# Performance work log

Hardware: AMD Instinct MI355X
Metric: run time of the kernel (lower is better)

Reference implementation:

```python
import jax, jax.numpy as jnp
import numpy as np

RADIUS = 5
WIN = (RADIUS - 1) * 2 + 1  # 9


def setup_inputs() -> dict:
    key = jax.random.key(0)
    k1, k2 = jax.random.split(key)
    B, K, H, W = 4, 4, 224, 224
    seg = jax.random.uniform(k1, (B, K, H, W), dtype=jnp.float32)
    weight = jax.random.uniform(k2, (B, 1, H, W, WIN, WIN), dtype=jnp.float32)
    return {"seg": seg, "weight": weight}


def reference(seg, weight):
    # seg: [B,K,H,W]; weight: [B,1,H,W,w,w] local affinity window, w = 2*(radius-1)+1
    B, K, H, W = seg.shape
    Kconst = jnp.float32(K)
    # torch pads by `radius` on all sides but only uses window offsets 0..2*(radius-1),
    # i.e. relative offsets [-radius, radius-2] -- replicate exactly.
    padded = jnp.pad(seg, ((0, 0), (0, 0), (RADIUS, RADIUS), (RADIUS, RADIUS)))
    # weighted sum over the local window without materializing [B,K,H,W,w,w]
    sum_w_seg = jnp.zeros_like(seg)
    for m in range(WIN):
        for n in range(WIN):
            sum_w_seg = sum_w_seg + padded[:, :, m:m + H, n:n + W] * weight[:, :, :, :, m, n]
    assocA = jnp.sum(sum_w_seg * seg, axis=(-1, -2))                      # [B,K]
    assocV = jnp.sum(jnp.sum(weight, axis=(-1, -2)) * seg, axis=(-1, -2))  # [B,K]
    assoc = jnp.sum(assocA / assocV, axis=-1)                              # [B]
    return jnp.sum(Kconst - assoc)
```

## Files before the change

### kernel.cpp

```cpp
#include <hip/hip_runtime.h>

#define RADIUS 5
#define WIN 9
#define BB 4
#define KK 4
#define HH 224
#define WW 224
#define HW (HH * WW)
#define PD 234
#define PAREA (PD * PD)
#define NBUCKET 64
#define PARTIAL_FLOATS (NBUCKET * BB * 8)

#define PX_PER_BLOCK 64
#define BLOCKS_TOTAL (BB * HW / PX_PER_BLOCK)
#define WF4_PER_BLOCK (PX_PER_BLOCK * 81 / 4)


__global__ __launch_bounds__(256) void ncuts_pad(
    const float* __restrict__ seg, float4* __restrict__ pseg)
{
    const int tid = blockIdx.x * 256 + threadIdx.x;
    if (tid >= BB * PAREA) return;
    const int b  = tid / PAREA;
    const int rc = tid - b * PAREA;
    const int r  = rc / PD;
    const int c  = rc - r * PD;
    const int hh = r - RADIUS;
    const int ww = c - RADIUS;
    float4 v = {0.f, 0.f, 0.f, 0.f};
    if (hh >= 0 && hh < HH && ww >= 0 && ww < WW) {
        const float* sb = seg + (size_t)b * KK * HW + hh * WW + ww;
        v.x = sb[0 * HW];
        v.y = sb[1 * HW];
        v.z = sb[2 * HW];
        v.w = sb[3 * HW];
    }
    pseg[tid] = v;
}

template<int T0, int T1>
__device__ __forceinline__ void do_taps(const float* __restrict__ wl,
                                        const float4* __restrict__ pb, int roff,
                                        float& a0, float& a1, float& a2, float& a3,
                                        float& wsum)
{
    #pragma unroll
    for (int tap = T0; tap < T1; ++tap) {
        const int m = tap / 9;
        const int n = tap - 9 * m;
        const float wv = wl[tap];
        const float4 s = pb[roff + m * PD + n];
        a0 = fmaf(wv, s.x, a0);
        a1 = fmaf(wv, s.y, a1);
        a2 = fmaf(wv, s.z, a2);
        a3 = fmaf(wv, s.w, a3);
        wsum += wv;
    }
}

__global__ __launch_bounds__(256, 7) void ncuts_main(
    const float4* __restrict__ weight4,
    const float4* __restrict__ pseg,
    float* __restrict__ partial)
{
    __shared__ float wlds[PX_PER_BLOCK * 81];

    const int tid  = threadIdx.x;
    const int lane = tid & 63;
    const int ws   = tid >> 6;

    const float4* wsrc = weight4 + (size_t)blockIdx.x * WF4_PER_BLOCK;
    float4* wdst = (float4*)wlds;
    #pragma unroll
    for (int it = 0; it < 6; ++it) {
        const int idx = it * 256 + tid;
        if (idx < WF4_PER_BLOCK) wdst[idx] = wsrc[idx];
    }
    __syncthreads();

    const int px  = blockIdx.x * PX_PER_BLOCK + lane;
    const int b   = px / HW;
    const int rem = px - b * HW;
    const int h   = rem / WW;
    const int w   = rem - h * WW;
    const int roff = h * PD + w;

    const float4* pb = pseg + (size_t)b * PAREA;
    const float* wl  = &wlds[lane * 81];

    float a0 = 0.f, a1 = 0.f, a2 = 0.f, a3 = 0.f, wsum = 0.f;

    switch (ws) {
        case 0: do_taps< 0, 21>(wl, pb, roff, a0, a1, a2, a3, wsum); break;
        case 1: do_taps<21, 41>(wl, pb, roff, a0, a1, a2, a3, wsum); break;
        case 2: do_taps<41, 61>(wl, pb, roff, a0, a1, a2, a3, wsum); break;
        default: do_taps<61, 81>(wl, pb, roff, a0, a1, a2, a3, wsum); break;
    }

    const float4 o = pb[roff + RADIUS * PD + RADIUS];

    float vals[8] = { a0 * o.x, a1 * o.y, a2 * o.z, a3 * o.w,
                      wsum * o.x, wsum * o.y, wsum * o.z, wsum * o.w };

    #pragma unroll
    for (int i = 0; i < 8; ++i) {
        float v = vals[i];
        v += __shfl_down(v, 32);
        v += __shfl_down(v, 16);
        v += __shfl_down(v, 8);
        v += __shfl_down(v, 4);
        v += __shfl_down(v, 2);
        v += __shfl_down(v, 1);
        vals[i] = v;
    }

    if (lane == 0) {
        const int bucket = (blockIdx.x * 4 + ws) & (NBUCKET - 1);
        float* dst = partial + (bucket * BB + b) * 8;
        #pragma unroll
        for (int i = 0; i < 8; ++i)
            atomicAdd(dst + i, vals[i]);
    }
}

__global__ __launch_bounds__(64) void ncuts_final(
    const float* __restrict__ partial, float* __restrict__ out)
{
    __shared__ float sums[32];
    const int t = threadIdx.x;
    if (t < 32) {
        const int b = t >> 3;
        const int i = t & 7;
        float s = 0.f;
        for (int bucket = 0; bucket < NBUCKET; ++bucket)
            s += partial[(bucket * BB + b) * 8 + i];
        sums[b * 8 + i] = s;
    }
    __syncthreads();
    if (t == 0) {
        float total = 0.f;
        for (int b = 0; b < BB; ++b) {
            float assoc = 0.f;
            for (int k = 0; k < KK; ++k) {
                const float A = sums[b * 8 + k];
                const float V = sums[b * 8 + 4 + k];
                assoc += A / V;
            }
            total += (float)KK - assoc;
        }
        out[0] = total;
    }
}

extern "C" void kernel_launch(void* const* d_in, const int* in_sizes, int n_in,
                              void* d_out, int out_size, void* d_ws, size_t ws_size,
                              hipStream_t stream) {
    const float* seg     = (const float*)d_in[0];
    const float4* weight = (const float4*)d_in[1];
    float* out     = (float*)d_out;
    float* wsf     = (float*)d_ws;
    float* partial = wsf;
    float4* pseg   = (float4*)(wsf + PARTIAL_FLOATS);

    hipMemsetAsync(d_ws, 0, PARTIAL_FLOATS * sizeof(float), stream);

    {
        const int total = BB * PAREA;
        const int grid  = (total + 255) / 256;
        hipLaunchKernelGGL(ncuts_pad, dim3(grid), dim3(256), 0, stream, seg, pseg);
    }
    {
        hipLaunchKernelGGL(ncuts_main, dim3(BLOCKS_TOTAL), dim3(256), 0, stream,
                           weight, pseg, partial);
    }
    hipLaunchKernelGGL(ncuts_final, dim3(1), dim3(64), 0, stream, partial, out);
}
```

Baseline: 123.0 us.

## Fuse memset and final reduction into pad/main kernels; load weights via global_load_lds

Replaces the hipMemsetAsync with zeroing of the partial and counter buffers inside the pad kernel. The final reduction kernel becomes a last-block-done step in the main kernel, driven by an atomic counter and thread fences. Weight tiles are staged into LDS with direct global-to-LDS loads, which skip the register round trip. This cuts two launches or stream operations and some load overhead, at the cost of an extra atomic and fence in every block.

```diff
diff --git a/kernel.cpp b/kernel.cpp
--- a/kernel.cpp
+++ b/kernel.cpp
@@ -11,16 +11,19 @@
 #define PAREA (PD * PD)
 #define NBUCKET 64
 #define PARTIAL_FLOATS (NBUCKET * BB * 8)
+#define CTRL_FLOATS 2056
+#define PSEG_OFF 2560
 
 #define PX_PER_BLOCK 64
 #define BLOCKS_TOTAL (BB * HW / PX_PER_BLOCK)
 #define WF4_PER_BLOCK (PX_PER_BLOCK * 81 / 4)
 
-
 __global__ __launch_bounds__(256) void ncuts_pad(
-    const float* __restrict__ seg, float4* __restrict__ pseg)
+    const float* __restrict__ seg, float4* __restrict__ pseg,
+    float* __restrict__ ctrl)
 {
     const int tid = blockIdx.x * 256 + threadIdx.x;
+    if (tid < CTRL_FLOATS) ctrl[tid] = 0.0f;
     if (tid >= BB * PAREA) return;
     const int b  = tid / PAREA;
     const int rc = tid - b * PAREA;
@@ -62,21 +65,30 @@
 __global__ __launch_bounds__(256, 7) void ncuts_main(
     const float4* __restrict__ weight4,
     const float4* __restrict__ pseg,
-    float* __restrict__ partial)
+    float* __restrict__ partial,
+    int* __restrict__ counter,
+    float* __restrict__ out)
 {
     __shared__ float wlds[PX_PER_BLOCK * 81];
+    __shared__ float xred[32];
+    __shared__ int lastflag;
 
     const int tid  = threadIdx.x;
     const int lane = tid & 63;
     const int ws   = tid >> 6;
 
     const float4* wsrc = weight4 + (size_t)blockIdx.x * WF4_PER_BLOCK;
-    float4* wdst = (float4*)wlds;
+    float4* wlds4 = (float4*)wlds;
     #pragma unroll
-    for (int it = 0; it < 6; ++it) {
-        const int idx = it * 256 + tid;
-        if (idx < WF4_PER_BLOCK) wdst[idx] = wsrc[idx];
+    for (int it = 0; it < 5; ++it) {
+        const int base = it * 256 + ws * 64;
+        __builtin_amdgcn_global_load_lds(
+            (const __attribute__((address_space(1))) void*)(wsrc + base + lane),
+            (__attribute__((address_space(3))) void*)(wlds4 + base),
+            16, 0, 0);
     }
+    if (tid < 16)
+        wlds4[1280 + tid] = wsrc[1280 + tid];
     __syncthreads();
 
     const int px  = blockIdx.x * PX_PER_BLOCK + lane;
@@ -122,31 +134,32 @@
         for (int i = 0; i < 8; ++i)
             atomicAdd(dst + i, vals[i]);
     }
-}
 
-__global__ __launch_bounds__(64) void ncuts_final(
-    const float* __restrict__ partial, float* __restrict__ out)
-{
-    __shared__ float sums[32];
-    const int t = threadIdx.x;
-    if (t < 32) {
-        const int b = t >> 3;
-        const int i = t & 7;
+    __threadfence();
+    if (tid == 0) {
+        const int c = atomicAdd(counter, 1);
+        lastflag = (c == BLOCKS_TOTAL - 1);
+    }
+    __syncthreads();
+    if (!lastflag) return;
+
+    __threadfence();
+    if (tid < 32) {
+        const int bb = tid >> 3;
+        const int i  = tid & 7;
         float s = 0.f;
         for (int bucket = 0; bucket < NBUCKET; ++bucket)
-            s += partial[(bucket * BB + b) * 8 + i];
-        sums[b * 8 + i] = s;
+            s += __hip_atomic_load(&partial[(bucket * BB + bb) * 8 + i],
+                                   __ATOMIC_RELAXED, __HIP_MEMORY_SCOPE_AGENT);
+        xred[bb * 8 + i] = s;
     }
     __syncthreads();
-    if (t == 0) {
+    if (tid == 0) {
         float total = 0.f;
-        for (int b = 0; b < BB; ++b) {
+        for (int bb = 0; bb < BB; ++bb) {
             float assoc = 0.f;
-            for (int k = 0; k < KK; ++k) {
-                const float A = sums[b * 8 + k];
-                const float V = sums[b * 8 + 4 + k];
-                assoc += A / V;
-            }
+            for (int k = 0; k < KK; ++k)
+                assoc += xred[bb * 8 + k] / xred[bb * 8 + 4 + k];
             total += (float)KK - assoc;
         }
         out[0] = total;
@@ -161,18 +174,15 @@
     float* out     = (float*)d_out;
     float* wsf     = (float*)d_ws;
     float* partial = wsf;
-    float4* pseg   = (float4*)(wsf + PARTIAL_FLOATS);
-
-    hipMemsetAsync(d_ws, 0, PARTIAL_FLOATS * sizeof(float), stream);
+    int*   counter = (int*)(wsf + 2048);
+    float4* pseg   = (float4*)(wsf + PSEG_OFF);
 
     {
         const int total = BB * PAREA;
         const int grid  = (total + 255) / 256;
-        hipLaunchKernelGGL(ncuts_pad, dim3(grid), dim3(256), 0, stream, seg, pseg);
+        hipLaunchKernelGGL(ncuts_pad, dim3(grid), dim3(256), 0, stream,
+                           seg, pseg, wsf);
     }
-    {
-        hipLaunchKernelGGL(ncuts_main, dim3(BLOCKS_TOTAL), dim3(256), 0, stream,
-                           weight, pseg, partial);
-    }
-    hipLaunchKernelGGL(ncuts_final, dim3(1), dim3(64), 0, stream, partial, out);
+    hipLaunchKernelGGL(ncuts_main, dim3(BLOCKS_TOTAL), dim3(256), 0, stream,
+                       weight, pseg, partial, counter, out);
 }
```

After: 378.5 us. 208% more time.
